# Performance work log

Measured on AMD Instinct MI355X. Metric: run time of the kernel, lower is better.

## Reference

```python
import jax, jax.numpy as jnp
import numpy as np

N_NODES = 100000
N_EDGES = 3200000
N_FEAT = 128
N_GRAPHS = 256
N_CLASSES = 10


def setup_inputs() -> dict:
    key = jax.random.key(0)
    ks = jax.random.split(key, 10)
    x = jax.random.normal(ks[0], (N_NODES, N_FEAT), dtype=jnp.float32)
    edge_index = jax.random.randint(ks[1], (2, N_EDGES), 0, N_NODES, dtype=jnp.int64)
    batch = jnp.sort(jax.random.randint(ks[2], (N_NODES,), 0, N_GRAPHS, dtype=jnp.int64))
    # GCNConv weights (glorot-ish scaling) and biases
    W1 = jax.random.normal(ks[3], (N_FEAT, 16), dtype=jnp.float32) / np.sqrt(N_FEAT)
    b1 = jnp.zeros((16,), dtype=jnp.float32)
    W2 = jax.random.normal(ks[4], (16, 32), dtype=jnp.float32) / np.sqrt(16.0)
    b2 = jnp.zeros((32,), dtype=jnp.float32)
    Wfc = jax.random.normal(ks[5], (32, N_CLASSES), dtype=jnp.float32) / np.sqrt(32.0)
    bfc = jnp.zeros((N_CLASSES,), dtype=jnp.float32)
    return {"x": x, "edge_index": edge_index, "batch": batch,
            "W1": W1, "b1": b1, "W2": W2, "b2": b2, "Wfc": Wfc, "bfc": bfc}


def reference(x, edge_index, batch, W1, b1, W2, b2, Wfc, bfc):
    N = x.shape[0]
    # --- GCN normalization with self-loops (PyG GCNConv default) ---
    loop = jnp.arange(N, dtype=edge_index.dtype)
    src = jnp.concatenate([edge_index[0], loop])  # [E+N]
    dst = jnp.concatenate([edge_index[1], loop])  # [E+N]
    ones = jnp.ones_like(src, dtype=x.dtype)
    deg = jax.ops.segment_sum(ones, dst, num_segments=N)  # in-degree incl self-loop
    dinv = jax.lax.rsqrt(deg)  # deg >= 1 thanks to self-loops
    norm = dinv[src] * dinv[dst]  # [E+N]

    def gcn_conv(h, W, b):
        h = h @ W                               # [N, out] linear first (small out dim)
        msg = h[src] * norm[:, None]            # gather + edge-wise scale
        agg = jax.ops.segment_sum(msg, dst, num_segments=N)  # scatter-add
        return agg + b

    h = jax.nn.relu(gcn_conv(x, W1, b1))
    h = jax.nn.relu(gcn_conv(h, W2, b2))

    # --- global mean pool over graphs ---
    g_sum = jax.ops.segment_sum(h, batch, num_segments=N_GRAPHS)  # [G, 32]
    g_cnt = jax.ops.segment_sum(jnp.ones((N,), dtype=h.dtype), batch, num_segments=N_GRAPHS)
    pooled = g_sum / jnp.maximum(g_cnt, 1.0)[:, None]

    return pooled @ Wfc + bfc  # [G, num_classes]
```

## Files before the change

### kernel.cpp

```cpp
#include <hip/hip_runtime.h>
#include <hip/hip_fp16.h>

#define NF   128
#define C1   16
#define C2   32
#define NCLS 10
#define BSH  8
#define BN   256
#define MAXB 512
#define S    9216
#define TILE 4096
#define CAP  12288


__global__ __launch_bounds__(512) void k_bin(const int* __restrict__ ei,
                                             int* __restrict__ packed,
                                             int* __restrict__ offmat,
                                             int E, int nbuck) {
    __shared__ int hist[MAXB];
    __shared__ int off0[MAXB];
    __shared__ int cur[MAXB];
    int tid = threadIdx.x;
    long long t0 = (long long)blockIdx.x * TILE;

    for (int i = tid; i < MAXB; i += 512) hist[i] = 0;
    __syncthreads();

    long long eb = t0 + (long long)tid * 8;
    int src[8], dst[8];
    if (eb + 8 <= E) {
        const int4* s4 = (const int4*)(ei + eb);
        const int4* d4 = (const int4*)(ei + E + eb);
        int4 a = s4[0], b = s4[1], c = d4[0], d = d4[1];
        src[0]=a.x; src[1]=a.y; src[2]=a.z; src[3]=a.w;
        src[4]=b.x; src[5]=b.y; src[6]=b.z; src[7]=b.w;
        dst[0]=c.x; dst[1]=c.y; dst[2]=c.z; dst[3]=c.w;
        dst[4]=d.x; dst[5]=d.y; dst[6]=d.z; dst[7]=d.w;
    } else {
#pragma unroll
        for (int u = 0; u < 8; ++u) {
            long long e = eb + u;
            src[u] = (e < E) ? ei[e] : 0;
            dst[u] = (e < E) ? ei[E + e] : -1;
        }
    }
#pragma unroll
    for (int u = 0; u < 8; ++u)
        if (dst[u] >= 0) atomicAdd(&hist[dst[u] >> BSH], 1);
    __syncthreads();
    if (tid < 64) {
        int carry = 0;
        for (int c = 0; c < MAXB / 64; ++c) {
            int idx = c * 64 + tid;
            int v = hist[idx];
            int orig = v;
            for (int off = 1; off < 64; off <<= 1) {
                int t = __shfl_up(v, off);
                if (tid >= off) v += t;
            }
            int ex = v - orig + carry;
            off0[idx] = ex;
            cur[idx] = ex;
            carry += __shfl(v, 63);
        }
    }
    __syncthreads();
    int* orow = offmat + (size_t)blockIdx.x * (nbuck + 1);
    for (int b = tid; b <= nbuck; b += 512) orow[b] = off0[b];
#pragma unroll
    for (int u = 0; u < 8; ++u) {
        int d = dst[u];
        if (d >= 0) {
            int b = d >> BSH;
            int slot = atomicAdd(&cur[b], 1);
            packed[t0 + slot] = src[u] | ((d & (BN - 1)) << 17);
        }
    }
}


__global__ __launch_bounds__(1024) void k_csr(const int* __restrict__ packed,
                                              const int* __restrict__ offmat,
                                              int* __restrict__ csr,
                                              int* __restrict__ rowptr,
                                              int* __restrict__ deg,
                                              float* __restrict__ dinv,
                                              int N, int nbuck, int nblkA) {
    __shared__ int stage[CAP];
    __shared__ int startA[1024];
    __shared__ int o1A[1024];
    __shared__ int hcnt[BN];
    __shared__ int cur[BN];
    __shared__ int wsum[16];
    __shared__ int woff[4];
    int tid = threadIdx.x;
    int wid = tid >> 6, lane = tid & 63;
    int b = blockIdx.x;
    size_t base = (size_t)b * S;

    int len = 0, o1 = 0;
    if (tid < nblkA) {
        const int* orow = offmat + (size_t)tid * (nbuck + 1) + b;
        o1 = orow[0];
        len = orow[1] - o1;
    }
    o1A[tid] = o1;
    if (tid < BN) hcnt[tid] = 0;

    int v = len;
#pragma unroll
    for (int off = 1; off < 64; off <<= 1) {
        int t = __shfl_up(v, off);
        if (lane >= off) v += t;
    }
    if (lane == 63) wsum[wid] = v;
    __syncthreads();
    if (tid < 16) {
        int w = wsum[tid];
#pragma unroll
        for (int off = 1; off < 16; off <<= 1) {
            int t = __shfl_up(w, off);
            if (tid >= off) w += t;
        }
        wsum[tid] = w;
    }
    __syncthreads();
    int m = wsum[15];
    int incl = v + ((wid > 0) ? wsum[wid - 1] : 0);
    startA[tid] = incl - len;
    __syncthreads();
    if (m > CAP) m = CAP;

    for (int i = tid; i < m; i += 1024) {
        int lo = 0, hi = 1023;
        while (lo < hi) {
            int mid = (lo + hi + 1) >> 1;
            if (startA[mid] <= i) lo = mid; else hi = mid - 1;
        }
        int p = packed[(size_t)lo * TILE + o1A[lo] + (i - startA[lo])];
        stage[i] = p;
        atomicAdd(&hcnt[p >> 17], 1);
    }
    __syncthreads();
    int v2 = (tid < BN) ? hcnt[tid] : 0;
    int s2 = v2;
#pragma unroll
    for (int off = 1; off < 64; off <<= 1) {
        int t = __shfl_up(s2, off);
        if (lane >= off) s2 += t;
    }
    if (tid < BN && lane == 63) wsum[wid] = s2;
    __syncthreads();
    if (tid == 0) {
        int acc = 0;
#pragma unroll
        for (int k = 0; k < 4; ++k) { int t = wsum[k]; woff[k] = acc; acc += t; }
    }
    __syncthreads();
    if (tid < BN) {
        int ex = (s2 - v2) + woff[wid];
        cur[tid] = ex;
        int n = (b << BSH) + tid;
        if (n < N) {
            rowptr[n] = (int)base + ex;
            deg[n] = v2;
            dinv[n] = rsqrtf((float)v2 + 1.0f);
        }
    }
    __syncthreads();
    for (int i = tid; i < m; i += 1024) {
        int p = stage[i];
        int slot = atomicAdd(&cur[p >> 17], 1);
        csr[base + slot] = p & 0x1FFFF;
    }
}


__global__ __launch_bounds__(256) void k_lin1(const float* __restrict__ x,
                                              const float* __restrict__ W1,
                                              const float* __restrict__ dinv,
                                              __half* __restrict__ y1h, int N) {
    __shared__ float ws[NF * C1];
    __shared__ float xs[16 * 132];
    int tid = threadIdx.x;
    for (int t = tid; t < NF * C1; t += 256) ws[t] = W1[t];
    int n0 = blockIdx.x * 16;
    const float4* x4 = (const float4*)x;
    for (int t = tid; t < 16 * 32; t += 256) {
        int r = t >> 5, c = t & 31;
        int n = n0 + r;
        float4 v = (n < N) ? x4[(size_t)n * 32 + c] : make_float4(0.f, 0.f, 0.f, 0.f);
        float* d = &xs[r * 132 + c * 4];
        d[0] = v.x; d[1] = v.y; d[2] = v.z; d[3] = v.w;
    }
    __syncthreads();
    int r = tid >> 4, j = tid & 15;
    float acc = 0.0f;
#pragma unroll 4
    for (int k = 0; k < NF; ++k) acc += xs[r * 132 + k] * ws[k * C1 + j];
    int n = n0 + r;
    if (n < N) y1h[(size_t)n * C1 + j] = __float2half_rn(acc * dinv[n]);
}


template <int MODE>
__global__ __launch_bounds__(256) void k_gather_h(const int* __restrict__ rowptr,
                                                  const int* __restrict__ deg,
                                                  const int* __restrict__ csr,
                                                  const float* __restrict__ dinv,
                                                  const float* __restrict__ bias,
                                                  const uint2* __restrict__ yh,
                                                  void* __restrict__ outp, int N) {
    int tid = threadIdx.x;
    int j = tid & 3;
    int n = blockIdx.x * 64 + (tid >> 2);
    if (n >= N) return;
    int k0 = rowptr[n];
    int k1 = k0 + deg[n];
    union U { uint2 u; __half2 h[2]; };
    U su; su.u = yh[(size_t)n * 4 + j];
    float2 sl = __half22float2(su.h[0]), shh = __half22float2(su.h[1]);
    float a0 = sl.x, a1 = sl.y, a2 = shh.x, a3 = shh.y;
    float b0 = 0.f, b1v = 0.f, b2 = 0.f, b3 = 0.f;
    int k = k0;
    for (; k + 3 < k1; k += 4) {
        int s0 = csr[k], s1 = csr[k + 1], s2 = csr[k + 2], s3 = csr[k + 3];
        U v0, v1, v2, v3;
        v0.u = yh[(size_t)s0 * 4 + j];
        v1.u = yh[(size_t)s1 * 4 + j];
        v2.u = yh[(size_t)s2 * 4 + j];
        v3.u = yh[(size_t)s3 * 4 + j];
        float2 l0 = __half22float2(v0.h[0]), h0 = __half22float2(v0.h[1]);
        float2 l1 = __half22float2(v1.h[0]), h1 = __half22float2(v1.h[1]);
        float2 l2 = __half22float2(v2.h[0]), h2 = __half22float2(v2.h[1]);
        float2 l3 = __half22float2(v3.h[0]), h3 = __half22float2(v3.h[1]);
        a0 += l0.x; a1 += l0.y; a2 += h0.x; a3 += h0.y;
        b0 += l1.x; b1v += l1.y; b2 += h1.x; b3 += h1.y;
        a0 += l2.x; a1 += l2.y; a2 += h2.x; a3 += h2.y;
        b0 += l3.x; b1v += l3.y; b2 += h3.x; b3 += h3.y;
    }
    for (; k < k1; ++k) {
        U v; v.u = yh[(size_t)csr[k] * 4 + j];
        float2 l = __half22float2(v.h[0]), h = __half22float2(v.h[1]);
        a0 += l.x; a1 += l.y; a2 += h.x; a3 += h.y;
    }
    float dn = dinv[n];
    float r0 = dn * (a0 + b0), r1 = dn * (a1 + b1v);
    float r2 = dn * (a2 + b2), r3 = dn * (a3 + b3);
    if (MODE == 0) {
        ((float4*)outp)[(size_t)n * 4 + j] = make_float4(r0, r1, r2, r3);
    } else {
        float4 bb = ((const float4*)bias)[j];
        U o;
        o.h[0] = __floats2half2_rn(fmaxf(r0 + bb.x, 0.0f) * dn, fmaxf(r1 + bb.y, 0.0f) * dn);
        o.h[1] = __floats2half2_rn(fmaxf(r2 + bb.z, 0.0f) * dn, fmaxf(r3 + bb.w, 0.0f) * dn);
        ((uint2*)outp)[(size_t)n * 4 + j] = o.u;
    }
}


__global__ __launch_bounds__(256) void k_pool_fc(const float* __restrict__ z,
                                                 const float* __restrict__ W2,
                                                 const float* __restrict__ b2,
                                                 const int* __restrict__ batch,
                                                 const float* __restrict__ Wfc,
                                                 const float* __restrict__ bfc,
                                                 float* __restrict__ out, int N, int G) {
    __shared__ float W2s[C1 * C2];
    int tid = threadIdx.x;
    for (int t = tid; t < C1 * C2; t += 256) W2s[t] = W2[t];

    int g = blockIdx.x;
    int lo = 0, hi = N;
    while (lo < hi) { int m = (lo + hi) >> 1; if (batch[m] < g) lo = m + 1; else hi = m; }
    int start = lo;
    lo = start; hi = N;
    while (lo < hi) { int m = (lo + hi) >> 1; if (batch[m] < g + 1) lo = m + 1; else hi = m; }
    int end = lo;
    __syncthreads();

    int i = tid & 31, r = tid >> 5;
    float bi = b2[i];
    float acc = 0.0f;
    for (int n = start + r; n < end; n += 8) {
        const float* zr = &z[(size_t)n * C1];
        float h = bi;
#pragma unroll
        for (int j = 0; j < C1; ++j) h += zr[j] * W2s[j * C2 + i];
        acc += fmaxf(h, 0.0f);
    }

    __shared__ float red[256];
    red[tid] = acc;
    __syncthreads();
    for (int s = 4; s >= 1; s >>= 1) {
        if (r < s) red[tid] += red[tid + s * 32];
        __syncthreads();
    }
    __shared__ float pooled[C2];
    if (tid < C2) {
        float cnt = (float)(end - start);
        pooled[tid] = red[tid] / fmaxf(cnt, 1.0f);
    }
    __syncthreads();
    if (tid < NCLS) {
        float a = bfc[tid];
#pragma unroll
        for (int j = 0; j < C2; ++j) a += pooled[j] * Wfc[j * NCLS + tid];
        out[g * NCLS + tid] = a;
    }
}

extern "C" void kernel_launch(void* const* d_in, const int* in_sizes, int n_in,
                              void* d_out, int out_size, void* d_ws, size_t ws_size,
                              hipStream_t stream) {
    const float* x    = (const float*)d_in[0];
    const int*   ei   = (const int*)d_in[1];
    const int*   batch= (const int*)d_in[2];
    const float* W1   = (const float*)d_in[3];
    const float* b1   = (const float*)d_in[4];
    const float* W2   = (const float*)d_in[5];
    const float* b2   = (const float*)d_in[6];
    const float* Wfc  = (const float*)d_in[7];
    const float* bfc  = (const float*)d_in[8];
    float* out = (float*)d_out;

    const int N = in_sizes[0] / NF;
    const int E = in_sizes[1] / 2;
    const int G = out_size / NCLS;
    const int nbuck = (N + BN - 1) >> BSH;
    const int nblkA = (E + TILE - 1) / TILE;

    char* p = (char*)d_ws;
    auto alloc = [&](size_t bytes) { char* q = p; p += (bytes + 63) & ~(size_t)63; return q; };
    int*     rowptr  = (int*)    alloc((size_t)N * 4);
    int*     deg     = (int*)    alloc((size_t)N * 4);
    float*   dinv    = (float*)  alloc((size_t)N * 4);
    int*     packed  = (int*)    alloc((size_t)nblkA * TILE * 4);
    int*     offmat  = (int*)    alloc((size_t)nblkA * (nbuck + 1) * 4);
    int*     csr     = (int*)    alloc((size_t)nbuck * S * 4);
    __half*  y1h     = (__half*) alloc((size_t)N * C1 * 2);
    __half*  uh      = (__half*) alloc((size_t)N * C1 * 2);
    float*   z       = (float*)  alloc((size_t)N * C1 * 4);

    const int B = 256;

    k_bin<<<nblkA, 512, 0, stream>>>(ei, packed, offmat, E, nbuck);
    k_csr<<<nbuck, 1024, 0, stream>>>(packed, offmat, csr, rowptr, deg, dinv,
                                      N, nbuck, nblkA);

    k_lin1<<<(N + 15) / 16, B, 0, stream>>>(x, W1, dinv, y1h, N);
    k_gather_h<1><<<(N + 63) / 64, B, 0, stream>>>(rowptr, deg, csr, dinv, b1,
                                                   (const uint2*)y1h, uh, N);
    k_gather_h<0><<<(N + 63) / 64, B, 0, stream>>>(rowptr, deg, csr, dinv, b1,
                                                   (const uint2*)uh, z, N);

    k_pool_fc<<<G, B, 0, stream>>>(z, W2, b2, batch, Wfc, bfc, out, N, G);
}
```

Baseline: 171.6 us.

## Fuse linear1 into CSR build and second aggregation into pooling

Moves the first linear layer into the CSR construction kernel, reusing its shared stage buffer and per-bucket dinv values, so a separate launch is no longer needed. The second gather now applies W2, bias and ReLU in registers and accumulates per-graph sums in shared memory before flushing them with global atomics. This removes the z intermediate and the per-graph pooling scan. A small final kernel then divides by counts and applies the FC layer. Risks are the extra serial work in the 1024-thread CSR blocks, atomic contention on g_sum, and the shared slot array assuming each 64-node block spans at most 64 graphs.

Result: slower. 176.7 us (+3.0%).

```diff
diff --git a/kernel.cpp b/kernel.cpp
--- a/kernel.cpp
+++ b/kernel.cpp
@@ -85,12 +85,17 @@
                                               int* __restrict__ rowptr,
                                               int* __restrict__ deg,
                                               float* __restrict__ dinv,
+                                              const float* __restrict__ x,
+                                              const float* __restrict__ W1,
+                                              __half* __restrict__ y1h,
+                                              float* __restrict__ g_sum,
                                               int N, int nbuck, int nblkA) {
     __shared__ int stage[CAP];
     __shared__ int startA[1024];
     __shared__ int o1A[1024];
     __shared__ int hcnt[BN];
     __shared__ int cur[BN];
+    __shared__ float fdinv[BN];
     __shared__ int wsum[16];
     __shared__ int woff[4];
     int tid = threadIdx.x;
@@ -98,6 +103,8 @@
     int b = blockIdx.x;
     size_t base = (size_t)b * S;
 
+    if (b < 8) g_sum[b * 1024 + tid] = 0.0f;
+
     int len = 0, o1 = 0;
     if (tid < nblkA) {
         const int* orow = offmat + (size_t)tid * (nbuck + 1) + b;
@@ -160,11 +167,13 @@
     if (tid < BN) {
         int ex = (s2 - v2) + woff[wid];
         cur[tid] = ex;
+        float dv = rsqrtf((float)v2 + 1.0f);
+        fdinv[tid] = dv;
         int n = (b << BSH) + tid;
         if (n < N) {
             rowptr[n] = (int)base + ex;
             deg[n] = v2;
-            dinv[n] = rsqrtf((float)v2 + 1.0f);
+            dinv[n] = dv;
         }
     }
     __syncthreads();
@@ -173,44 +182,41 @@
         int slot = atomicAdd(&cur[p >> 17], 1);
         csr[base + slot] = p & 0x1FFFF;
     }
-}
-
-
-__global__ __launch_bounds__(256) void k_lin1(const float* __restrict__ x,
-                                              const float* __restrict__ W1,
-                                              const float* __restrict__ dinv,
-                                              __half* __restrict__ y1h, int N) {
-    __shared__ float ws[NF * C1];
-    __shared__ float xs[16 * 132];
-    int tid = threadIdx.x;
-    for (int t = tid; t < NF * C1; t += 256) ws[t] = W1[t];
-    int n0 = blockIdx.x * 16;
+    __syncthreads();
+
+    float* Wl = (float*)stage;
+    float* xt = Wl + 2048;
+    for (int t = tid; t < NF * C1; t += 1024) Wl[t] = W1[t];
+    int n0b = b << BSH;
     const float4* x4 = (const float4*)x;
-    for (int t = tid; t < 16 * 32; t += 256) {
-        int r = t >> 5, c = t & 31;
-        int n = n0 + r;
-        float4 v = (n < N) ? x4[(size_t)n * 32 + c] : make_float4(0.f, 0.f, 0.f, 0.f);
-        float* d = &xs[r * 132 + c * 4];
-        d[0] = v.x; d[1] = v.y; d[2] = v.z; d[3] = v.w;
-    }
-    __syncthreads();
-    int r = tid >> 4, j = tid & 15;
-    float acc = 0.0f;
+    for (int iter = 0; iter < 4; ++iter) {
+        int r0n = n0b + iter * 64;
+        __syncthreads();
+        for (int t = tid; t < 64 * 32; t += 1024) {
+            int r = t >> 5, c = t & 31;
+            int n = r0n + r;
+            float4 vv = (n < N) ? x4[(size_t)n * 32 + c] : make_float4(0.f, 0.f, 0.f, 0.f);
+            float* dp = &xt[r * 132 + c * 4];
+            dp[0] = vv.x; dp[1] = vv.y; dp[2] = vv.z; dp[3] = vv.w;
+        }
+        __syncthreads();
+        int r = tid >> 4, j = tid & 15;
+        float acc = 0.0f;
 #pragma unroll 4
-    for (int k = 0; k < NF; ++k) acc += xs[r * 132 + k] * ws[k * C1 + j];
-    int n = n0 + r;
-    if (n < N) y1h[(size_t)n * C1 + j] = __float2half_rn(acc * dinv[n]);
-}
-
-
-template <int MODE>
-__global__ __launch_bounds__(256) void k_gather_h(const int* __restrict__ rowptr,
-                                                  const int* __restrict__ deg,
-                                                  const int* __restrict__ csr,
-                                                  const float* __restrict__ dinv,
-                                                  const float* __restrict__ bias,
-                                                  const uint2* __restrict__ yh,
-                                                  void* __restrict__ outp, int N) {
+        for (int k = 0; k < NF; ++k) acc += xt[r * 132 + k] * Wl[k * C1 + j];
+        int n = r0n + r;
+        if (n < N) y1h[(size_t)n * C1 + j] = __float2half_rn(acc * fdinv[iter * 64 + r]);
+    }
+}
+
+
+__global__ __launch_bounds__(256) void k_gather1(const int* __restrict__ rowptr,
+                                                 const int* __restrict__ deg,
+                                                 const int* __restrict__ csr,
+                                                 const float* __restrict__ dinv,
+                                                 const float* __restrict__ bias,
+                                                 const uint2* __restrict__ yh,
+                                                 uint2* __restrict__ outp, int N) {
     int tid = threadIdx.x;
     int j = tid & 3;
     int n = blockIdx.x * 64 + (tid >> 2);
@@ -247,67 +253,123 @@
     float dn = dinv[n];
     float r0 = dn * (a0 + b0), r1 = dn * (a1 + b1v);
     float r2 = dn * (a2 + b2), r3 = dn * (a3 + b3);
-    if (MODE == 0) {
-        ((float4*)outp)[(size_t)n * 4 + j] = make_float4(r0, r1, r2, r3);
-    } else {
-        float4 bb = ((const float4*)bias)[j];
-        U o;
-        o.h[0] = __floats2half2_rn(fmaxf(r0 + bb.x, 0.0f) * dn, fmaxf(r1 + bb.y, 0.0f) * dn);
-        o.h[1] = __floats2half2_rn(fmaxf(r2 + bb.z, 0.0f) * dn, fmaxf(r3 + bb.w, 0.0f) * dn);
-        ((uint2*)outp)[(size_t)n * 4 + j] = o.u;
-    }
-}
-
-
-__global__ __launch_bounds__(256) void k_pool_fc(const float* __restrict__ z,
-                                                 const float* __restrict__ W2,
-                                                 const float* __restrict__ b2,
-                                                 const int* __restrict__ batch,
-                                                 const float* __restrict__ Wfc,
-                                                 const float* __restrict__ bfc,
-                                                 float* __restrict__ out, int N, int G) {
+    float4 bb = ((const float4*)bias)[j];
+    U o;
+    o.h[0] = __floats2half2_rn(fmaxf(r0 + bb.x, 0.0f) * dn, fmaxf(r1 + bb.y, 0.0f) * dn);
+    o.h[1] = __floats2half2_rn(fmaxf(r2 + bb.z, 0.0f) * dn, fmaxf(r3 + bb.w, 0.0f) * dn);
+    outp[(size_t)n * 4 + j] = o.u;
+}
+
+
+__global__ __launch_bounds__(256) void k_gather_pool(const int* __restrict__ rowptr,
+                                                     const int* __restrict__ deg,
+                                                     const int* __restrict__ csr,
+                                                     const float* __restrict__ dinv,
+                                                     const float* __restrict__ W2,
+                                                     const float* __restrict__ b2,
+                                                     const int* __restrict__ batch,
+                                                     const uint2* __restrict__ yh,
+                                                     float* __restrict__ g_sum, int N) {
     __shared__ float W2s[C1 * C2];
+    __shared__ float acc[64 * C2];
     int tid = threadIdx.x;
     for (int t = tid; t < C1 * C2; t += 256) W2s[t] = W2[t];
-
-    int g = blockIdx.x;
+    for (int t = tid; t < 64 * C2; t += 256) acc[t] = 0.0f;
+
+    int n0 = blockIdx.x * 64;
+    int g_lo = batch[min(n0, N - 1)];
+    int g_hi = batch[min(n0 + 63, N - 1)];
+    __syncthreads();
+
+    int j = tid & 3;
+    int n = n0 + (tid >> 2);
+    if (n < N) {
+        int k0 = rowptr[n];
+        int k1 = k0 + deg[n];
+        union U { uint2 u; __half2 h[2]; };
+        U su; su.u = yh[(size_t)n * 4 + j];
+        float2 sl = __half22float2(su.h[0]), shh = __half22float2(su.h[1]);
+        float a0 = sl.x, a1 = sl.y, a2 = shh.x, a3 = shh.y;
+        float b0 = 0.f, b1v = 0.f, b2v = 0.f, b3 = 0.f;
+        int k = k0;
+        for (; k + 3 < k1; k += 4) {
+            int s0 = csr[k], s1 = csr[k + 1], s2 = csr[k + 2], s3 = csr[k + 3];
+            U v0, v1, v2, v3;
+            v0.u = yh[(size_t)s0 * 4 + j];
+            v1.u = yh[(size_t)s1 * 4 + j];
+            v2.u = yh[(size_t)s2 * 4 + j];
+            v3.u = yh[(size_t)s3 * 4 + j];
+            float2 l0 = __half22float2(v0.h[0]), h0 = __half22float2(v0.h[1]);
+            float2 l1 = __half22float2(v1.h[0]), h1 = __half22float2(v1.h[1]);
+            float2 l2 = __half22float2(v2.h[0]), h2 = __half22float2(v2.h[1]);
+            float2 l3 = __half22float2(v3.h[0]), h3 = __half22float2(v3.h[1]);
+            a0 += l0.x; a1 += l0.y; a2 += h0.x; a3 += h0.y;
+            b0 += l1.x; b1v += l1.y; b2v += h1.x; b3 += h1.y;
+            a0 += l2.x; a1 += l2.y; a2 += h2.x; a3 += h2.y;
+            b0 += l3.x; b1v += l3.y; b2v += h3.x; b3 += h3.y;
+        }
+        for (; k < k1; ++k) {
+            U v; v.u = yh[(size_t)csr[k] * 4 + j];
+            float2 l = __half22float2(v.h[0]), h = __half22float2(v.h[1]);
+            a0 += l.x; a1 += l.y; a2 += h.x; a3 += h.y;
+        }
+        float dn = dinv[n];
+        float z0 = dn * (a0 + b0), z1 = dn * (a1 + b1v);
+        float z2 = dn * (a2 + b2v), z3 = dn * (a3 + b3);
+
+        float p[C2];
+        const float* w0 = &W2s[(4 * j + 0) * C2];
+        const float* w1 = &W2s[(4 * j + 1) * C2];
+        const float* w2 = &W2s[(4 * j + 2) * C2];
+        const float* w3 = &W2s[(4 * j + 3) * C2];
+#pragma unroll
+        for (int i = 0; i < C2; ++i)
+            p[i] = z0 * w0[i] + z1 * w1[i] + z2 * w2[i] + z3 * w3[i];
+#pragma unroll
+        for (int i = 0; i < C2; ++i) {
+            p[i] += __shfl_xor(p[i], 1);
+            p[i] += __shfl_xor(p[i], 2);
+        }
+        int g = batch[n];
+        float* arow = &acc[(g - g_lo) * C2];
+#pragma unroll
+        for (int i = 0; i < 8; ++i) {
+            int c = j * 8 + i;
+            atomicAdd(&arow[c], fmaxf(p[c] + b2[c], 0.0f));
+        }
+    }
+    __syncthreads();
+    int nslots = g_hi - g_lo + 1;
+    for (int t = tid; t < nslots * C2; t += 256) {
+        int s = t >> 5, c = t & 31;
+        float v = acc[s * C2 + c];
+        if (v != 0.0f) atomicAdd(&g_sum[(size_t)(g_lo + s) * C2 + c], v);
+    }
+}
+
+
+__global__ __launch_bounds__(256) void k_final(const float* __restrict__ g_sum,
+                                               const int* __restrict__ batch,
+                                               const float* __restrict__ Wfc,
+                                               const float* __restrict__ bfc,
+                                               float* __restrict__ out, int N, int G) {
+    int g = threadIdx.x;
+    if (g >= G) return;
     int lo = 0, hi = N;
     while (lo < hi) { int m = (lo + hi) >> 1; if (batch[m] < g) lo = m + 1; else hi = m; }
     int start = lo;
     lo = start; hi = N;
     while (lo < hi) { int m = (lo + hi) >> 1; if (batch[m] < g + 1) lo = m + 1; else hi = m; }
-    int end = lo;
-    __syncthreads();
-
-    int i = tid & 31, r = tid >> 5;
-    float bi = b2[i];
-    float acc = 0.0f;
-    for (int n = start + r; n < end; n += 8) {
-        const float* zr = &z[(size_t)n * C1];
-        float h = bi;
-#pragma unroll
-        for (int j = 0; j < C1; ++j) h += zr[j] * W2s[j * C2 + i];
-        acc += fmaxf(h, 0.0f);
-    }
-
-    __shared__ float red[256];
-    red[tid] = acc;
-    __syncthreads();
-    for (int s = 4; s >= 1; s >>= 1) {
-        if (r < s) red[tid] += red[tid + s * 32];
-        __syncthreads();
-    }
-    __shared__ float pooled[C2];
-    if (tid < C2) {
-        float cnt = (float)(end - start);
-        pooled[tid] = red[tid] / fmaxf(cnt, 1.0f);
-    }
-    __syncthreads();
-    if (tid < NCLS) {
-        float a = bfc[tid];
-#pragma unroll
-        for (int j = 0; j < C2; ++j) a += pooled[j] * Wfc[j * NCLS + tid];
-        out[g * NCLS + tid] = a;
+    float inv = 1.0f / fmaxf((float)(lo - start), 1.0f);
+    float pooled[C2];
+#pragma unroll
+    for (int jj = 0; jj < C2; ++jj) pooled[jj] = g_sum[(size_t)g * C2 + jj] * inv;
+#pragma unroll
+    for (int c = 0; c < NCLS; ++c) {
+        float a = bfc[c];
+#pragma unroll
+        for (int jj = 0; jj < C2; ++jj) a += pooled[jj] * Wfc[jj * NCLS + c];
+        out[g * NCLS + c] = a;
     }
 }
 
@@ -341,19 +403,15 @@
     int*     csr     = (int*)    alloc((size_t)nbuck * S * 4);
     __half*  y1h     = (__half*) alloc((size_t)N * C1 * 2);
     __half*  uh      = (__half*) alloc((size_t)N * C1 * 2);
-    float*   z       = (float*)  alloc((size_t)N * C1 * 4);
-
-    const int B = 256;
+    float*   g_sum   = (float*)  alloc((size_t)G * C2 * 4);
 
     k_bin<<<nblkA, 512, 0, stream>>>(ei, packed, offmat, E, nbuck);
     k_csr<<<nbuck, 1024, 0, stream>>>(packed, offmat, csr, rowptr, deg, dinv,
-                                      N, nbuck, nblkA);
-
-    k_lin1<<<(N + 15) / 16, B, 0, stream>>>(x, W1, dinv, y1h, N);
-    k_gather_h<1><<<(N + 63) / 64, B, 0, stream>>>(rowptr, deg, csr, dinv, b1,
-                                                   (const uint2*)y1h, uh, N);
-    k_gather_h<0><<<(N + 63) / 64, B, 0, stream>>>(rowptr, deg, csr, dinv, b1,
-                                                   (const uint2*)uh, z, N);
-
-    k_pool_fc<<<G, B, 0, stream>>>(z, W2, b2, batch, Wfc, bfc, out, N, G);
-}
+                                      x, W1, y1h, g_sum, N, nbuck, nblkA);
+
+    k_gather1<<<(N + 63) / 64, 256, 0, stream>>>(rowptr, deg, csr, dinv, b1,
+                                                 (const uint2*)y1h, (uint2*)uh, N);
+    k_gather_pool<<<(N + 63) / 64, 256, 0, stream>>>(rowptr, deg, csr, dinv, W2, b2,
+                                                     batch, (const uint2*)uh, g_sum, N);
+    k_final<<<1, 256, 0, stream>>>(g_sum, batch, Wfc, bfc, out, N, G);
+}
```
